# Optimization experiments

Measured on AMD Instinct MI355X. Metric: run time of the kernel, lower is better.

The kernel has to match this reference:

```python
import jax, jax.numpy as jnp
import numpy as np

EMBED_DIM = 1024
NUM_HEADS = 16
HEAD_DIM = EMBED_DIM // NUM_HEADS
B, T = 4, 2048


def setup_inputs() -> dict:
    key = jax.random.key(0)
    ks = jax.random.split(key, 5)
    s = 1.0 / np.sqrt(EMBED_DIM)
    x = jax.random.normal(ks[0], (B, T, EMBED_DIM), dtype=jnp.float32)
    W_qkv = jax.random.uniform(ks[1], (EMBED_DIM, 3 * EMBED_DIM), minval=-s, maxval=s, dtype=jnp.float32)
    b_qkv = jax.random.uniform(ks[2], (3 * EMBED_DIM,), minval=-s, maxval=s, dtype=jnp.float32)
    W_proj = jax.random.uniform(ks[3], (EMBED_DIM, EMBED_DIM), minval=-s, maxval=s, dtype=jnp.float32)
    b_proj = jax.random.uniform(ks[4], (EMBED_DIM,), minval=-s, maxval=s, dtype=jnp.float32)
    return {"x": x, "W_qkv": W_qkv, "b_qkv": b_qkv, "W_proj": W_proj, "b_proj": b_proj}


def reference(x, W_qkv, b_qkv, W_proj, b_proj):
    Bq, Tq, C = x.shape
    H, D = NUM_HEADS, HEAD_DIM
    qkv = x @ W_qkv + b_qkv                      # [B,T,3C]
    qkv = qkv.reshape(Bq, Tq, 3, H, D)
    q = qkv[:, :, 0].transpose(0, 2, 1, 3)       # [B,H,T,D]
    k = qkv[:, :, 1].transpose(0, 2, 1, 3)
    v = qkv[:, :, 2].transpose(0, 2, 1, 3)
    scale = 1.0 / jnp.sqrt(jnp.asarray(D, x.dtype))
    attn = jnp.einsum('bhqd,bhkd->bhqk', q, k) * scale  # [B,H,T,T]
    mask = jnp.tril(jnp.ones((Tq, Tq), dtype=bool))     # causal: keep lower triangle
    attn = jnp.where(mask, attn, jnp.asarray(-jnp.inf, attn.dtype))
    attn = jax.nn.softmax(attn, axis=-1)
    out = jnp.einsum('bhqk,bhkd->bhqd', attn, v)        # [B,H,T,D]
    out = out.transpose(0, 2, 1, 3).reshape(Bq, Tq, C)
    return out @ W_proj + b_proj
```

## Files before the change

kernel.cpp:

```cpp
#include <hip/hip_runtime.h>
#include <stdint.h>

typedef unsigned short ushort_t;
typedef __attribute__((ext_vector_type(4))) unsigned int  u32x4;
typedef __attribute__((ext_vector_type(2))) unsigned int  u32x2;
typedef __attribute__((ext_vector_type(4))) float         f32x4;
typedef __attribute__((ext_vector_type(8))) __bf16        bf16x8;
typedef __attribute__((ext_vector_type(2))) __bf16        bf16x2;

__device__ __forceinline__ ushort_t f2bf(float f) {
    unsigned int u = __float_as_uint(f);
    u += 0x7fffu + ((u >> 16) & 1u);
    return (ushort_t)(u >> 16);
}
__device__ __forceinline__ unsigned int pack2bf(float a, float b) {
    return (unsigned int)f2bf(a) | ((unsigned int)f2bf(b) << 16);
}
#if __has_builtin(__builtin_amdgcn_cvt_pk_bf16_f32)
__device__ __forceinline__ unsigned int pack2bf_fast(float a, float b) {
    bf16x2 v = __builtin_amdgcn_cvt_pk_bf16_f32(a, b);
    return __builtin_bit_cast(unsigned int, v);
}
#else
__device__ __forceinline__ unsigned int pack2bf_fast(float a, float b) {
    return pack2bf(a, b);
}
#endif
__device__ __forceinline__ f32x4 mfma16(bf16x8 a, bf16x8 b, f32x4 c) {
    return __builtin_amdgcn_mfma_f32_16x16x32_bf16(a, b, c, 0, 0, 0);
}
__device__ __forceinline__ bf16x8 ldfrag(const ushort_t* p) {
    return __builtin_bit_cast(bf16x8, *(const u32x4*)p);
}

#define QSCALE 0.18033688011112042f

__global__ __launch_bounds__(256) void xcast(const float* __restrict__ X,
                                             ushort_t* __restrict__ Xb) {
    long i = ((long)blockIdx.x * 256 + threadIdx.x) * 8;
    float4 a = *(const float4*)(X + i);
    float4 b = *(const float4*)(X + i + 4);
    u32x4 pk;
    pk.x = pack2bf(a.x, a.y); pk.y = pack2bf(a.z, a.w);
    pk.z = pack2bf(b.x, b.y); pk.w = pack2bf(b.z, b.w);
    *(u32x4*)(Xb + i) = pk;
}

__global__ __launch_bounds__(256) void wt_kernel(const float* __restrict__ W,
                                                 ushort_t* __restrict__ Wt,
                                                 int K, int N) {
    __shared__ float tile[32][33];
    int tx = threadIdx.x, ty = threadIdx.y;
    int n0 = blockIdx.x * 32, k0 = blockIdx.y * 32;
    for (int p = 0; p < 4; ++p)
        tile[ty + 8*p][tx] = W[(long)(k0 + ty + 8*p) * N + n0 + tx];
    __syncthreads();
    for (int p = 0; p < 4; ++p)
        Wt[(long)(n0 + ty + 8*p) * K + k0 + tx] = f2bf(tile[tx][ty + 8*p]);
}

__global__ __launch_bounds__(256) void gemm_qkv(const ushort_t* __restrict__ Xb,
                                                const ushort_t* __restrict__ Wt,
                                                const float* __restrict__ bias,
                                                ushort_t* __restrict__ Qo,
                                                ushort_t* __restrict__ Ko,
                                                ushort_t* __restrict__ Vto) {
    __shared__ __align__(16) ushort_t smem[128 * 136];

    const int tid  = threadIdx.x;
    const int g    = blockIdx.x;
    const int grp  = g / 192, rr = g % 192;
    const int m0   = (grp * 8 + (rr & 7)) * 128;
    const int n0   = (rr >> 3) * 128;
    const int lane = tid & 63, w = tid >> 6;
    const int quad = lane >> 4, l16 = lane & 15;
    const int wm = (w >> 1) * 64, wn = (w & 1) * 64;

    const int srow  = tid >> 2;
    const int slot  = tid & 3;
    const int oct   = slot ^ ((tid >> 3) & 3);
    const int wofs  = srow * 32 + slot * 8;
    const int rslot = (quad ^ ((l16 >> 1) & 3)) * 8;

    const ushort_t* Ap = Xb + (long)(m0 + srow) * 1024 + oct * 8;
    const ushort_t* Bp = Wt + (long)(n0 + srow) * 1024 + oct * 8;

    f32x4 acc[4][4] = {};

    u32x4 AA0 = *(const u32x4*)(Ap);
    u32x4 AA1 = *(const u32x4*)(Ap + 65536);
    u32x4 BA0 = *(const u32x4*)(Bp);
    u32x4 BA1 = *(const u32x4*)(Bp + 65536);
    u32x4 AB0 = *(const u32x4*)(Ap + 32);
    u32x4 AB1 = *(const u32x4*)(Ap + 32 + 65536);
    u32x4 BB0 = *(const u32x4*)(Bp + 32);
    u32x4 BB1 = *(const u32x4*)(Bp + 32 + 65536);

    for (int k0 = 0; k0 < 1024; k0 += 64) {
        {
            ushort_t* As = smem;
            ushort_t* Bs = smem + 8192;
            *(u32x4*)&As[wofs]        = AA0;
            *(u32x4*)&As[wofs + 2048] = AA1;
            *(u32x4*)&Bs[wofs]        = BA0;
            *(u32x4*)&Bs[wofs + 2048] = BA1;
            int kf = (k0 + 64 < 1024) ? k0 + 64 : k0;
            AA0 = *(const u32x4*)(Ap + kf);
            AA1 = *(const u32x4*)(Ap + kf + 65536);
            BA0 = *(const u32x4*)(Bp + kf);
            BA1 = *(const u32x4*)(Bp + kf + 65536);
            __syncthreads();
            bf16x8 af[4], bfr[4];
            for (int i = 0; i < 4; ++i)
                af[i] = ldfrag(&As[(wm + 16*i + l16) * 32 + rslot]);
            for (int j = 0; j < 4; ++j)
                bfr[j] = ldfrag(&Bs[(wn + 16*j + l16) * 32 + rslot]);
            for (int i = 0; i < 4; ++i)
                for (int j = 0; j < 4; ++j)
                    acc[i][j] = mfma16(af[i], bfr[j], acc[i][j]);
        }
        {
            ushort_t* As = smem + 4096;
            ushort_t* Bs = smem + 8192 + 4096;
            *(u32x4*)&As[wofs]        = AB0;
            *(u32x4*)&As[wofs + 2048] = AB1;
            *(u32x4*)&Bs[wofs]        = BB0;
            *(u32x4*)&Bs[wofs + 2048] = BB1;
            int kf = (k0 + 96 < 1024) ? k0 + 96 : k0 + 32;
            AB0 = *(const u32x4*)(Ap + kf);
            AB1 = *(const u32x4*)(Ap + kf + 65536);
            BB0 = *(const u32x4*)(Bp + kf);
            BB1 = *(const u32x4*)(Bp + kf + 65536);
            __syncthreads();
            bf16x8 af[4], bfr[4];
            for (int i = 0; i < 4; ++i)
                af[i] = ldfrag(&As[(wm + 16*i + l16) * 32 + rslot]);
            for (int j = 0; j < 4; ++j)
                bfr[j] = ldfrag(&Bs[(wn + 16*j + l16) * 32 + rslot]);
            for (int i = 0; i < 4; ++i)
                for (int j = 0; j < 4; ++j)
                    acc[i][j] = mfma16(af[i], bfr[j], acc[i][j]);
        }
    }

    float bj[4];
    for (int j = 0; j < 4; ++j) bj[j] = bias[n0 + wn + 16*j + l16];
    const int bb = m0 >> 11, t0m = m0 & 2047;
    __syncthreads();

    if (n0 < 2048) {
        ushort_t* dst = (n0 < 1024) ? Qo : Ko;
        const float scale = (n0 < 1024) ? QSCALE : 1.0f;
        const int nbase = (n0 < 1024) ? n0 : n0 - 1024;
        for (int i = 0; i < 4; ++i)
            for (int j = 0; j < 4; ++j) {
                int nl = wn + 16*j + l16;
                for (int r = 0; r < 4; ++r) {
                    int ml = wm + 16*i + quad*4 + r;
                    smem[ml * 136 + nl] = f2bf((acc[i][j][r] + bj[j]) * scale);
                }
            }
        __syncthreads();
        for (int c = 0; c < 8; ++c) {
            int chunk = tid + 256 * c;
            int row = chunk >> 4, nc = (chunk & 15) * 8;
            int n = nbase + nc;
            int hh = n >> 6, d = n & 63;
            *(u32x4*)&dst[((long)(bb*16 + hh) * 2048 + t0m + row) * 64 + d] =
                *(const u32x4*)&smem[row * 136 + nc];
        }
    } else {
        for (int i = 0; i < 4; ++i)
            for (int j = 0; j < 4; ++j) {
                int nl = wn + 16*j + l16;
                for (int r = 0; r < 4; ++r) {
                    int ml = wm + 16*i + quad*4 + r;
                    smem[nl * 136 + ml] = f2bf(acc[i][j][r] + bj[j]);
                }
            }
        __syncthreads();
        for (int c = 0; c < 8; ++c) {
            int chunk = tid + 256 * c;
            int row = chunk >> 4, mc = (chunk & 15) * 8;
            int n = n0 - 2048 + row;
            int hh = n >> 6, d = n & 63;
            *(u32x4*)&Vto[((long)(bb*16 + hh) * 64 + d) * 2048 + t0m + mc] =
                *(const u32x4*)&smem[row * 136 + mc];
        }
    }
}

__global__ __launch_bounds__(256) void attn_kernel(const ushort_t* __restrict__ Q,
                                                   const ushort_t* __restrict__ K,
                                                   const ushort_t* __restrict__ Vt,
                                                   ushort_t* __restrict__ O) {
    __shared__ __align__(16) ushort_t Ks[2][64 * 64];
    __shared__ __align__(16) ushort_t Vs[2][64 * 64];
    __shared__ __align__(16) ushort_t Ps[128 * 72];

    const int tid  = threadIdx.x;
    const int lane = tid & 63, w = tid >> 6, quad = lane >> 4, l16 = lane & 15;
    const int g    = blockIdx.x;
    const int bh   = (g & 7) + 8 * ((g >> 3) & 7);
    const int p    = g >> 6;
    const ushort_t* qptr = Q  + (long)bh * 2048 * 64;
    const ushort_t* kptr = K  + (long)bh * 2048 * 64;
    const ushort_t* vptr = Vt + (long)bh * 64 * 2048;
    const int bb2 = bh >> 4, h = bh & 15;

    const int srow = tid >> 3;
    const int slot = tid & 7;
    const int oct  = slot ^ (srow & 7);
    const int koff = srow * 64 + oct * 8;
    const int voff = srow * 2048 + oct * 8;
    const int wofs = srow * 64 + slot * 8;

    for (int ti = 0; ti < 2; ++ti) {
        const int qt = ti ? (15 - p) : p;
        const int qbase = qt * 128;
        const int nkt = 2 * qt + 2;

        __syncthreads();
        for (int c = 0; c < 4; ++c) {
            int flat = tid + 256 * c;
            int row = flat >> 3, kc = (flat & 7) * 8;
            *(u32x4*)&Ps[row * 72 + kc] = *(const u32x4*)&qptr[(long)(qbase + row) * 64 + kc];
        }
        __syncthreads();
        bf16x8 qf[2][2];
        for (int nt = 0; nt < 2; ++nt)
            for (int kk = 0; kk < 2; ++kk)
                qf[nt][kk] = ldfrag(&Ps[(32*w + 16*nt + l16) * 72 + kk*32 + quad*8]);

        f32x4 acc[2][4] = {};
        float l_run[2] = {0.f, 0.f};

        auto phase = [&](int kt, ushort_t* Kb, ushort_t* Vb) {
            const int kbase = kt * 64;
            if (kbase > qbase + 32*w + 31) return;
            f32x4 s[4][2] = {};
            for (int kk = 0; kk < 2; ++kk)
                for (int mt = 0; mt < 4; ++mt) {
                    bf16x8 kf = ldfrag(&Kb[(16*mt + l16) * 64 + ((4*kk + quad) ^ (l16 & 7)) * 8]);
                    for (int nt = 0; nt < 2; ++nt)
                        s[mt][nt] = mfma16(kf, qf[nt][kk], s[mt][nt]);
                }
            if (kbase + 63 > qbase + 32*w) {
                for (int mt = 0; mt < 4; ++mt)
                    for (int nt = 0; nt < 2; ++nt) {
                        int qv = qbase + 32*w + 16*nt + l16;
                        for (int r = 0; r < 4; ++r)
                            if (kbase + 16*mt + 4*quad + r > qv)
                                s[mt][nt][r] = -__builtin_inff();
                    }
            }
            for (int nt = 0; nt < 2; ++nt)
                for (int mt = 0; mt < 4; ++mt) {
                    float p0 = __builtin_amdgcn_exp2f(s[mt][nt][0]);
                    float p1 = __builtin_amdgcn_exp2f(s[mt][nt][1]);
                    float p2 = __builtin_amdgcn_exp2f(s[mt][nt][2]);
                    float p3 = __builtin_amdgcn_exp2f(s[mt][nt][3]);
                    l_run[nt] += (p0 + p1) + (p2 + p3);
                    u32x2 pk;
                    pk.x = pack2bf_fast(p0, p1);
                    pk.y = pack2bf_fast(p2, p3);
                    *(u32x2*)&Ps[(32*w + 16*nt + l16) * 72 + 16*mt + 4*quad] = pk;
                }
            for (int kk = 0; kk < 2; ++kk) {
                bf16x8 pf0 = ldfrag(&Ps[(32*w + l16) * 72 + kk*32 + quad*8]);
                bf16x8 pf1 = ldfrag(&Ps[(32*w + 16 + l16) * 72 + kk*32 + quad*8]);
                for (int jd = 0; jd < 4; ++jd) {
                    bf16x8 vf = ldfrag(&Vb[(16*jd + l16) * 64 + ((4*kk + quad) ^ (l16 & 7)) * 8]);
                    acc[0][jd] = mfma16(pf0, vf, acc[0][jd]);
                    acc[1][jd] = mfma16(pf1, vf, acc[1][jd]);
                }
            }
        };

        u32x4 KA0 = *(const u32x4*)(kptr + koff);
        u32x4 KA1 = *(const u32x4*)(kptr + koff + 2048);
        u32x4 VA0 = *(const u32x4*)(vptr + voff);
        u32x4 VA1 = *(const u32x4*)(vptr + voff + 65536);
        u32x4 KB0 = *(const u32x4*)(kptr + 4096 + koff);
        u32x4 KB1 = *(const u32x4*)(kptr + 4096 + koff + 2048);
        u32x4 VB0 = *(const u32x4*)(vptr + 64 + voff);
        u32x4 VB1 = *(const u32x4*)(vptr + 64 + voff + 65536);

        for (int kt = 0; kt < nkt; kt += 2) {
            {
                *(u32x4*)&Ks[0][wofs]        = KA0;
                *(u32x4*)&Ks[0][wofs + 2048] = KA1;
                *(u32x4*)&Vs[0][wofs]        = VA0;
                *(u32x4*)&Vs[0][wofs + 2048] = VA1;
                int kf = (kt + 2 < nkt) ? kt + 2 : kt;
                KA0 = *(const u32x4*)(kptr + kf*4096 + koff);
                KA1 = *(const u32x4*)(kptr + kf*4096 + koff + 2048);
                VA0 = *(const u32x4*)(vptr + kf*64 + voff);
                VA1 = *(const u32x4*)(vptr + kf*64 + voff + 65536);
                __syncthreads();
                phase(kt, Ks[0], Vs[0]);
            }
            {
                *(u32x4*)&Ks[1][wofs]        = KB0;
                *(u32x4*)&Ks[1][wofs + 2048] = KB1;
                *(u32x4*)&Vs[1][wofs]        = VB0;
                *(u32x4*)&Vs[1][wofs + 2048] = VB1;
                int kf = (kt + 3 < nkt) ? kt + 3 : kt + 1;
                KB0 = *(const u32x4*)(kptr + kf*4096 + koff);
                KB1 = *(const u32x4*)(kptr + kf*4096 + koff + 2048);
                VB0 = *(const u32x4*)(vptr + kf*64 + voff);
                VB1 = *(const u32x4*)(vptr + kf*64 + voff + 65536);
                __syncthreads();
                phase(kt + 1, Ks[1], Vs[1]);
            }
        }

        for (int i = 0; i < 2; ++i) {
            float l = l_run[i];
            l += __shfl_xor(l, 16, 64);
            l += __shfl_xor(l, 32, 64);
            for (int r = 0; r < 4; ++r) {
                float linv = 1.0f / __shfl(l, (lane & 48) | (4*quad + r), 64);
                int t = qbase + 32*w + 16*i + 4*quad + r;
                for (int jd = 0; jd < 4; ++jd) {
                    int d = 16*jd + l16;
                    O[((long)(bb2*2048 + t)) * 1024 + h*64 + d] = f2bf(acc[i][jd][r] * linv);
                }
            }
        }
    }
}

__global__ __launch_bounds__(256) void gemm_proj(const ushort_t* __restrict__ A,
                                                 const ushort_t* __restrict__ Wt,
                                                 const float* __restrict__ bias,
                                                 float* __restrict__ Out) {
    __shared__ __align__(16) ushort_t smem[4 * 4096];

    const int tid  = threadIdx.x;
    const int g    = blockIdx.x;
    const int grp  = g / 64, rr = g % 64;
    const int m0   = (grp * 8 + (rr & 7)) * 128;
    const int n0   = (rr >> 3) * 128;
    const int lane = tid & 63, w = tid >> 6;
    const int quad = lane >> 4, l16 = lane & 15;
    const int wm = (w >> 1) * 64, wn = (w & 1) * 64;

    const int srow  = tid >> 2;
    const int slot  = tid & 3;
    const int oct   = slot ^ ((tid >> 3) & 3);
    const int wofs  = srow * 32 + slot * 8;
    const int rslot = (quad ^ ((l16 >> 1) & 3)) * 8;

    const ushort_t* Ap = A  + (long)(m0 + srow) * 1024 + oct * 8;
    const ushort_t* Bp = Wt + (long)(n0 + srow) * 1024 + oct * 8;

    f32x4 acc[4][4] = {};

    u32x4 AA0 = *(const u32x4*)(Ap);
    u32x4 AA1 = *(const u32x4*)(Ap + 65536);
    u32x4 BA0 = *(const u32x4*)(Bp);
    u32x4 BA1 = *(const u32x4*)(Bp + 65536);
    u32x4 AB0 = *(const u32x4*)(Ap + 32);
    u32x4 AB1 = *(const u32x4*)(Ap + 32 + 65536);
    u32x4 BB0 = *(const u32x4*)(Bp + 32);
    u32x4 BB1 = *(const u32x4*)(Bp + 32 + 65536);

    for (int k0 = 0; k0 < 1024; k0 += 64) {
        {
            ushort_t* As = smem;
            ushort_t* Bs = smem + 8192;
            *(u32x4*)&As[wofs]        = AA0;
            *(u32x4*)&As[wofs + 2048] = AA1;
            *(u32x4*)&Bs[wofs]        = BA0;
            *(u32x4*)&Bs[wofs + 2048] = BA1;
            int kf = (k0 + 64 < 1024) ? k0 + 64 : k0;
            AA0 = *(const u32x4*)(Ap + kf);
            AA1 = *(const u32x4*)(Ap + kf + 65536);
            BA0 = *(const u32x4*)(Bp + kf);
            BA1 = *(const u32x4*)(Bp + kf + 65536);
            __syncthreads();
            bf16x8 af[4], bfr[4];
            for (int i = 0; i < 4; ++i)
                af[i] = ldfrag(&As[(wm + 16*i + l16) * 32 + rslot]);
            for (int j = 0; j < 4; ++j)
                bfr[j] = ldfrag(&Bs[(wn + 16*j + l16) * 32 + rslot]);
            for (int i = 0; i < 4; ++i)
                for (int j = 0; j < 4; ++j)
                    acc[i][j] = mfma16(af[i], bfr[j], acc[i][j]);
        }
        {
            ushort_t* As = smem + 4096;
            ushort_t* Bs = smem + 8192 + 4096;
            *(u32x4*)&As[wofs]        = AB0;
            *(u32x4*)&As[wofs + 2048] = AB1;
            *(u32x4*)&Bs[wofs]        = BB0;
            *(u32x4*)&Bs[wofs + 2048] = BB1;
            int kf = (k0 + 96 < 1024) ? k0 + 96 : k0 + 32;
            AB0 = *(const u32x4*)(Ap + kf);
            AB1 = *(const u32x4*)(Ap + kf + 65536);
            BB0 = *(const u32x4*)(Bp + kf);
            BB1 = *(const u32x4*)(Bp + kf + 65536);
            __syncthreads();
            bf16x8 af[4], bfr[4];
            for (int i = 0; i < 4; ++i)
                af[i] = ldfrag(&As[(wm + 16*i + l16) * 32 + rslot]);
            for (int j = 0; j < 4; ++j)
                bfr[j] = ldfrag(&Bs[(wn + 16*j + l16) * 32 + rslot]);
            for (int i = 0; i < 4; ++i)
                for (int j = 0; j < 4; ++j)
                    acc[i][j] = mfma16(af[i], bfr[j], acc[i][j]);
        }
    }

    float bj[4];
    for (int j = 0; j < 4; ++j) bj[j] = bias[n0 + wn + 16*j + l16];
    for (int i = 0; i < 4; ++i)
        for (int j = 0; j < 4; ++j)
            for (int r = 0; r < 4; ++r) {
                int m = m0 + wm + 16*i + quad*4 + r;
                int n = n0 + wn + 16*j + l16;
                Out[(long)m * 1024 + n] = acc[i][j][r] + bj[j];
            }
}

extern "C" void kernel_launch(void* const* d_in, const int* in_sizes, int n_in,
                              void* d_out, int out_size, void* d_ws, size_t ws_size,
                              hipStream_t stream) {
    const float* x     = (const float*)d_in[0];
    const float* Wqkv  = (const float*)d_in[1];
    const float* bqkv  = (const float*)d_in[2];
    const float* Wproj = (const float*)d_in[3];
    const float* bproj = (const float*)d_in[4];
    float* out = (float*)d_out;

    ushort_t* wqkvt  = (ushort_t*)d_ws;
    ushort_t* wprojt = wqkvt  + 3072 * 1024;
    ushort_t* Qb     = wprojt + 1024 * 1024;
    ushort_t* Kb     = Qb  + 8388608;
    ushort_t* Vtb    = Kb  + 8388608;
    ushort_t* XbA2   = Vtb + 8388608;

    xcast<<<4096, 256, 0, stream>>>(x, XbA2);
    wt_kernel<<<dim3(96, 32), dim3(32, 8), 0, stream>>>(Wqkv, wqkvt, 1024, 3072);
    wt_kernel<<<dim3(32, 32), dim3(32, 8), 0, stream>>>(Wproj, wprojt, 1024, 1024);
    gemm_qkv<<<1536, 256, 0, stream>>>(XbA2, wqkvt, bqkv, Qb, Kb, Vtb);
    attn_kernel<<<512, 256, 0, stream>>>(Qb, Kb, Vtb, XbA2);
    gemm_proj<<<512, 256, 0, stream>>>(XbA2, wprojt, bproj, out);
}
```

Measured before the change: 244.7 us.

## Launch one attention block per query tile, longest tiles first

The attention kernel used to pair query tiles p and 15-p inside one block to balance causal work across 512 blocks. It now launches 1024 blocks, one per (batch-head, query tile), ordered so the longest query tiles are scheduled first, which relies on the hardware scheduler for load balance and raises parallelism. Address arithmetic for the K/V/P fragment loads is also hoisted into precomputed base pointers and column offsets. The trade-off is more block launches and more repeated Q loads and prologues, against fewer serial tiles per block.

Result: slower. 253.3 us (+3.5%).

```diff
diff --git a/kernel.cpp b/kernel.cpp
--- a/kernel.cpp
+++ b/kernel.cpp
@@ -201,8 +201,10 @@
     const int tid  = threadIdx.x;
     const int lane = tid & 63, w = tid >> 6, quad = lane >> 4, l16 = lane & 15;
     const int g    = blockIdx.x;
-    const int bh   = (g & 7) + 8 * ((g >> 3) & 7);
-    const int p    = g >> 6;
+    const int qt   = 15 - (g >> 6);
+    const int bh   = g & 63;
+    const int qbase = qt * 128;
+    const int nkt  = 2 * qt + 2;
     const ushort_t* qptr = Q  + (long)bh * 2048 * 64;
     const ushort_t* kptr = K  + (long)bh * 2048 * 64;
     const ushort_t* vptr = Vt + (long)bh * 64 * 2048;
@@ -215,117 +217,131 @@
     const int voff = srow * 2048 + oct * 8;
     const int wofs = srow * 64 + slot * 8;
 
-    for (int ti = 0; ti < 2; ++ti) {
-        const int qt = ti ? (15 - p) : p;
-        const int qbase = qt * 128;
-        const int nkt = 2 * qt + 2;
-
-        __syncthreads();
-        for (int c = 0; c < 4; ++c) {
-            int flat = tid + 256 * c;
-            int row = flat >> 3, kc = (flat & 7) * 8;
-            *(u32x4*)&Ps[row * 72 + kc] = *(const u32x4*)&qptr[(long)(qbase + row) * 64 + kc];
-        }
-        __syncthreads();
-        bf16x8 qf[2][2];
+    const int kcol0 = (quad ^ (l16 & 7)) * 8;
+    const int kcol1 = ((4 + quad) ^ (l16 & 7)) * 8;
+    const ushort_t* kb0 = &Ks[0][l16 * 64];
+    const ushort_t* kb1 = &Ks[1][l16 * 64];
+    const ushort_t* vb0 = &Vs[0][l16 * 64];
+    const ushort_t* vb1 = &Vs[1][l16 * 64];
+    ushort_t* prow = &Ps[(32*w + l16) * 72];
+
+    for (int c = 0; c < 4; ++c) {
+        int flat = tid + 256 * c;
+        int row = flat >> 3, kc = (flat & 7) * 8;
+        *(u32x4*)&Ps[row * 72 + kc] = *(const u32x4*)&qptr[(long)(qbase + row) * 64 + kc];
+    }
+    __syncthreads();
+    bf16x8 qf[2][2];
+    for (int nt = 0; nt < 2; ++nt)
+        for (int kk = 0; kk < 2; ++kk)
+            qf[nt][kk] = ldfrag(&Ps[(32*w + 16*nt + l16) * 72 + kk*32 + quad*8]);
+
+    f32x4 acc[2][4] = {};
+    float l_run[2] = {0.f, 0.f};
+    const int qv0 = qbase + 32*w + l16;
+    const int keyl = 4*quad;
+
+    auto phase = [&](int kt, const ushort_t* kb, const ushort_t* vb) {
+        const int kbase = kt * 64;
+        if (kbase > qbase + 32*w + 31) return;
+        f32x4 s[4][2] = {};
+        for (int mt = 0; mt < 4; ++mt) {
+            bf16x8 kf = ldfrag(kb + mt*1024 + kcol0);
+            s[mt][0] = mfma16(kf, qf[0][0], s[mt][0]);
+            s[mt][1] = mfma16(kf, qf[1][0], s[mt][1]);
+        }
+        for (int mt = 0; mt < 4; ++mt) {
+            bf16x8 kf = ldfrag(kb + mt*1024 + kcol1);
+            s[mt][0] = mfma16(kf, qf[0][1], s[mt][0]);
+            s[mt][1] = mfma16(kf, qf[1][1], s[mt][1]);
+        }
+        if (kbase + 63 > qbase + 32*w) {
+            for (int mt = 0; mt < 4; ++mt) {
+                int key = kbase + 16*mt + keyl;
+                for (int r = 0; r < 4; ++r) {
+                    if (key + r > qv0)      s[mt][0][r] = -__builtin_inff();
+                    if (key + r > qv0 + 16) s[mt][1][r] = -__builtin_inff();
+                }
+            }
+        }
         for (int nt = 0; nt < 2; ++nt)
-            for (int kk = 0; kk < 2; ++kk)
-                qf[nt][kk] = ldfrag(&Ps[(32*w + 16*nt + l16) * 72 + kk*32 + quad*8]);
-
-        f32x4 acc[2][4] = {};
-        float l_run[2] = {0.f, 0.f};
-
-        auto phase = [&](int kt, ushort_t* Kb, ushort_t* Vb) {
-            const int kbase = kt * 64;
-            if (kbase > qbase + 32*w + 31) return;
-            f32x4 s[4][2] = {};
-            for (int kk = 0; kk < 2; ++kk)
-                for (int mt = 0; mt < 4; ++mt) {
-                    bf16x8 kf = ldfrag(&Kb[(16*mt + l16) * 64 + ((4*kk + quad) ^ (l16 & 7)) * 8]);
-                    for (int nt = 0; nt < 2; ++nt)
-                        s[mt][nt] = mfma16(kf, qf[nt][kk], s[mt][nt]);
-                }
-            if (kbase + 63 > qbase + 32*w) {
-                for (int mt = 0; mt < 4; ++mt)
-                    for (int nt = 0; nt < 2; ++nt) {
-                        int qv = qbase + 32*w + 16*nt + l16;
-                        for (int r = 0; r < 4; ++r)
-                            if (kbase + 16*mt + 4*quad + r > qv)
-                                s[mt][nt][r] = -__builtin_inff();
-                    }
-            }
-            for (int nt = 0; nt < 2; ++nt)
-                for (int mt = 0; mt < 4; ++mt) {
-                    float p0 = __builtin_amdgcn_exp2f(s[mt][nt][0]);
-                    float p1 = __builtin_amdgcn_exp2f(s[mt][nt][1]);
-                    float p2 = __builtin_amdgcn_exp2f(s[mt][nt][2]);
-                    float p3 = __builtin_amdgcn_exp2f(s[mt][nt][3]);
-                    l_run[nt] += (p0 + p1) + (p2 + p3);
-                    u32x2 pk;
-                    pk.x = pack2bf_fast(p0, p1);
-                    pk.y = pack2bf_fast(p2, p3);
-                    *(u32x2*)&Ps[(32*w + 16*nt + l16) * 72 + 16*mt + 4*quad] = pk;
-                }
-            for (int kk = 0; kk < 2; ++kk) {
-                bf16x8 pf0 = ldfrag(&Ps[(32*w + l16) * 72 + kk*32 + quad*8]);
-                bf16x8 pf1 = ldfrag(&Ps[(32*w + 16 + l16) * 72 + kk*32 + quad*8]);
-                for (int jd = 0; jd < 4; ++jd) {
-                    bf16x8 vf = ldfrag(&Vb[(16*jd + l16) * 64 + ((4*kk + quad) ^ (l16 & 7)) * 8]);
-                    acc[0][jd] = mfma16(pf0, vf, acc[0][jd]);
-                    acc[1][jd] = mfma16(pf1, vf, acc[1][jd]);
-                }
-            }
-        };
-
-        u32x4 KA0 = *(const u32x4*)(kptr + koff);
-        u32x4 KA1 = *(const u32x4*)(kptr + koff + 2048);
-        u32x4 VA0 = *(const u32x4*)(vptr + voff);
-        u32x4 VA1 = *(const u32x4*)(vptr + voff + 65536);
-        u32x4 KB0 = *(const u32x4*)(kptr + 4096 + koff);
-        u32x4 KB1 = *(const u32x4*)(kptr + 4096 + koff + 2048);
-        u32x4 VB0 = *(const u32x4*)(vptr + 64 + voff);
-        u32x4 VB1 = *(const u32x4*)(vptr + 64 + voff + 65536);
-
-        for (int kt = 0; kt < nkt; kt += 2) {
-            {
-                *(u32x4*)&Ks[0][wofs]        = KA0;
-                *(u32x4*)&Ks[0][wofs + 2048] = KA1;
-                *(u32x4*)&Vs[0][wofs]        = VA0;
-                *(u32x4*)&Vs[0][wofs + 2048] = VA1;
-                int kf = (kt + 2 < nkt) ? kt + 2 : kt;
-                KA0 = *(const u32x4*)(kptr + kf*4096 + koff);
-                KA1 = *(const u32x4*)(kptr + kf*4096 + koff + 2048);
-                VA0 = *(const u32x4*)(vptr + kf*64 + voff);
-                VA1 = *(const u32x4*)(vptr + kf*64 + voff + 65536);
-                __syncthreads();
-                phase(kt, Ks[0], Vs[0]);
-            }
-            {
-                *(u32x4*)&Ks[1][wofs]        = KB0;
-                *(u32x4*)&Ks[1][wofs + 2048] = KB1;
-                *(u32x4*)&Vs[1][wofs]        = VB0;
-                *(u32x4*)&Vs[1][wofs + 2048] = VB1;
-                int kf = (kt + 3 < nkt) ? kt + 3 : kt + 1;
-                KB0 = *(const u32x4*)(kptr + kf*4096 + koff);
-                KB1 = *(const u32x4*)(kptr + kf*4096 + koff + 2048);
-                VB0 = *(const u32x4*)(vptr + kf*64 + voff);
-                VB1 = *(const u32x4*)(vptr + kf*64 + voff + 65536);
-                __syncthreads();
-                phase(kt + 1, Ks[1], Vs[1]);
-            }
-        }
-
-        for (int i = 0; i < 2; ++i) {
-            float l = l_run[i];
-            l += __shfl_xor(l, 16, 64);
-            l += __shfl_xor(l, 32, 64);
-            for (int r = 0; r < 4; ++r) {
-                float linv = 1.0f / __shfl(l, (lane & 48) | (4*quad + r), 64);
-                int t = qbase + 32*w + 16*i + 4*quad + r;
-                for (int jd = 0; jd < 4; ++jd) {
-                    int d = 16*jd + l16;
-                    O[((long)(bb2*2048 + t)) * 1024 + h*64 + d] = f2bf(acc[i][jd][r] * linv);
-                }
+            for (int mt = 0; mt < 4; ++mt) {
+                float p0 = __builtin_amdgcn_exp2f(s[mt][nt][0]);
+                float p1 = __builtin_amdgcn_exp2f(s[mt][nt][1]);
+                float p2 = __builtin_amdgcn_exp2f(s[mt][nt][2]);
+                float p3 = __builtin_amdgcn_exp2f(s[mt][nt][3]);
+                l_run[nt] += (p0 + p1) + (p2 + p3);
+                u32x2 pk;
+                pk.x = pack2bf_fast(p0, p1);
+                pk.y = pack2bf_fast(p2, p3);
+                *(u32x2*)(prow + nt*1152 + 16*mt + keyl) = pk;
+            }
+        {
+            bf16x8 pf0 = ldfrag(prow + quad*8);
+            bf16x8 pf1 = ldfrag(prow + 1152 + quad*8);
+            for (int jd = 0; jd < 4; ++jd) {
+                bf16x8 vf = ldfrag(vb + jd*1024 + kcol0);
+                acc[0][jd] = mfma16(pf0, vf, acc[0][jd]);
+                acc[1][jd] = mfma16(pf1, vf, acc[1][jd]);
+            }
+            pf0 = ldfrag(prow + 32 + quad*8);
+            pf1 = ldfrag(prow + 1152 + 32 + quad*8);
+            for (int jd = 0; jd < 4; ++jd) {
+                bf16x8 vf = ldfrag(vb + jd*1024 + kcol1);
+                acc[0][jd] = mfma16(pf0, vf, acc[0][jd]);
+                acc[1][jd] = mfma16(pf1, vf, acc[1][jd]);
+            }
+        }
+    };
+
+    u32x4 KA0 = *(const u32x4*)(kptr + koff);
+    u32x4 KA1 = *(const u32x4*)(kptr + koff + 2048);
+    u32x4 VA0 = *(const u32x4*)(vptr + voff);
+    u32x4 VA1 = *(const u32x4*)(vptr + voff + 65536);
+    u32x4 KB0 = *(const u32x4*)(kptr + 4096 + koff);
+    u32x4 KB1 = *(const u32x4*)(kptr + 4096 + koff + 2048);
+    u32x4 VB0 = *(const u32x4*)(vptr + 64 + voff);
+    u32x4 VB1 = *(const u32x4*)(vptr + 64 + voff + 65536);
+
+    for (int kt = 0; kt < nkt; kt += 2) {
+        {
+            *(u32x4*)&Ks[0][wofs]        = KA0;
+            *(u32x4*)&Ks[0][wofs + 2048] = KA1;
+            *(u32x4*)&Vs[0][wofs]        = VA0;
+            *(u32x4*)&Vs[0][wofs + 2048] = VA1;
+            int kf = (kt + 2 < nkt) ? kt + 2 : kt;
+            KA0 = *(const u32x4*)(kptr + kf*4096 + koff);
+            KA1 = *(const u32x4*)(kptr + kf*4096 + koff + 2048);
+            VA0 = *(const u32x4*)(vptr + kf*64 + voff);
+            VA1 = *(const u32x4*)(vptr + kf*64 + voff + 65536);
+            __syncthreads();
+            phase(kt, kb0, vb0);
+        }
+        {
+            *(u32x4*)&Ks[1][wofs]        = KB0;
+            *(u32x4*)&Ks[1][wofs + 2048] = KB1;
+            *(u32x4*)&Vs[1][wofs]        = VB0;
+            *(u32x4*)&Vs[1][wofs + 2048] = VB1;
+            int kf = (kt + 3 < nkt) ? kt + 3 : kt + 1;
+            KB0 = *(const u32x4*)(kptr + kf*4096 + koff);
+            KB1 = *(const u32x4*)(kptr + kf*4096 + koff + 2048);
+            VB0 = *(const u32x4*)(vptr + kf*64 + voff);
+            VB1 = *(const u32x4*)(vptr + kf*64 + voff + 65536);
+            __syncthreads();
+            phase(kt + 1, kb1, vb1);
+        }
+    }
+
+    for (int i = 0; i < 2; ++i) {
+        float l = l_run[i];
+        l += __shfl_xor(l, 16, 64);
+        l += __shfl_xor(l, 32, 64);
+        for (int r = 0; r < 4; ++r) {
+            float linv = 1.0f / __shfl(l, (lane & 48) | (4*quad + r), 64);
+            int t = qbase + 32*w + 16*i + 4*quad + r;
+            for (int jd = 0; jd < 4; ++jd) {
+                int d = 16*jd + l16;
+                O[((long)(bb2*2048 + t)) * 1024 + h*64 + d] = f2bf(acc[i][jd][r] * linv);
             }
         }
     }
@@ -445,6 +461,6 @@
     wt_kernel<<<dim3(96, 32), dim3(32, 8), 0, stream>>>(Wqkv, wqkvt, 1024, 3072);
     wt_kernel<<<dim3(32, 32), dim3(32, 8), 0, stream>>>(Wproj, wprojt, 1024, 1024);
     gemm_qkv<<<1536, 256, 0, stream>>>(XbA2, wqkvt, bqkv, Qb, Kb, Vtb);
-    attn_kernel<<<512, 256, 0, stream>>>(Qb, Kb, Vtb, XbA2);
+    attn_kernel<<<1024, 256, 0, stream>>>(Qb, Kb, Vtb, XbA2);
     gemm_proj<<<512, 256, 0, stream>>>(XbA2, wprojt, bproj, out);
 }
```
